# Optimization experiments

Measured on AMD Instinct MI355X. Metric: run time of the kernel, lower is better.

The kernel has to match this reference:

```python
import jax, jax.numpy as jnp
import numpy as np
from jax import lax

N, C_IN, H, W = 32, 128, 64, 64
C_OUT, KH, KW = 256, 3, 3
C_DIM = 64


def setup_inputs() -> dict:
    key = jax.random.key(0)
    k1, k2, k3, k4, k5 = jax.random.split(key, 5)
    return {
        "x": jax.random.normal(k1, (N, C_IN, H, W), dtype=jnp.float32),
        "c": jax.random.normal(k2, (N, C_DIM), dtype=jnp.float32),
        "weight": jax.random.normal(k3, (C_OUT, C_IN, KH, KW), dtype=jnp.float32),
        "c_weight": jax.random.normal(k4, (C_OUT, C_DIM), dtype=jnp.float32),
        "bias": jax.random.normal(k5, (C_OUT,), dtype=jnp.float32),
    }


def reference(x, c, weight, c_weight, bias):
    # Equivalent to the module's unfold + matmul path (groups=1, dilation=1,
    # zero padding=1, stride=1): a direct conv fused with the spatially
    # invariant context bias c @ c_weight^T and the channel bias.
    out = lax.conv_general_dilated(
        x, weight,
        window_strides=(1, 1),
        padding=((1, 1), (1, 1)),
        dimension_numbers=("NCHW", "OIHW", "NCHW"),
    )  # (N, C_out, H, W)
    ctx = jnp.einsum("nd,od->no", c, c_weight)  # (N, C_out), same at every spatial loc
    return out + ctx[:, :, None, None] + bias[None, :, None, None]
```

## Files before the change

kernel.cpp:

```cpp
#include <hip/hip_runtime.h>
#include <hip/hip_bf16.h>


#define NN   32
#define CIN  128
#define HH   64
#define WW   64
#define COUT 256
#define CDIM 64

#define WT_BYTES  ((size_t)9*COUT*CIN*2)
#define CTX_BYTES ((size_t)NN*COUT*4)
#define WS_NEEDED (WT_BYTES + CTX_BYTES)

#define AROWS 264
#define ARSTR 136
#define ACHNK 4488

typedef __attribute__((ext_vector_type(8))) short short8;
typedef __attribute__((ext_vector_type(4))) float float4v;

#define SETPRIO(x) __builtin_amdgcn_s_setprio(x)

__global__ __launch_bounds__(256) void prep_wc(const float* __restrict__ wgt,
                                               const float* __restrict__ c,
                                               const float* __restrict__ cw,
                                               const float* __restrict__ bias,
                                               __hip_bfloat16* __restrict__ wT,
                                               float* __restrict__ ctx) {
    int bid = blockIdx.x;
    if (bid < 1152) {
        int idx = bid * 256 + threadIdx.x;
        int ci  = idx & 127;
        int co  = (idx >> 7) & 255;
        int tap = idx >> 15;
        wT[idx] = __float2bfloat16(wgt[((size_t)co * CIN + ci) * 9 + tap]);
    } else {
        int idx = (bid - 1152) * 256 + threadIdx.x;
        int co = idx & 255, n = idx >> 8;
        float a = bias[co];
        #pragma unroll 8
        for (int d = 0; d < CDIM; ++d) a += c[n * CDIM + d] * cw[co * CDIM + d];
        ctx[idx] = a;
    }
}

__global__ __launch_bounds__(512, 4) void conv_mfma(
    const float* __restrict__ x,
    const __hip_bfloat16* __restrict__ wT,
    const float* __restrict__ ctx,
    float* __restrict__ out)
{
    __shared__ __align__(16) short A_s[AROWS * ARSTR];

    int bid = blockIdx.x;
    int mt  = (bid & 7) * 128 + (bid >> 3);
    int n   = mt >> 5;
    int h0  = (mt & 31) << 1;

    int tid  = threadIdx.x;
    int lane = tid & 63, wv = tid >> 6;
    int wm = (wv & 1) * 64;
    int wn = (wv >> 1) * 64;
    int l15 = lane & 15, lu = lane >> 4;

    const __hip_bfloat16* wB = wT + ((size_t)(wn + l15) * CIN) + lu * 8;

    short8 bCur[4], bNxt[4];
    #pragma unroll
    for (int ni = 0; ni < 4; ++ni)
        bCur[ni] = *(const short8*)(wB + (size_t)ni * (16 * CIN));

    #pragma unroll
    for (int z = 0; z < 9; ++z) {
        int g = z * 512 + tid;
        if (g < ACHNK) *(short8*)&A_s[g * 8] = (short8){};
    }
    __syncthreads();

    int h0m1 = h0 - 1;
    #pragma unroll
    for (int i = 0; i < 8; ++i) {
        int task = wv * 8 + i;
        int hl   = task >> 4;
        int oct  = task & 15;
        int hh   = h0m1 + hl;
        if (hh >= 0 && hh < HH) {
            const float* src = x + (((size_t)(n * CIN + oct * 8)) * HH + hh) * WW + lane;
            union { short8 s; __hip_bfloat16 b[8]; } u;
            #pragma unroll
            for (int k = 0; k < 8; ++k)
                u.b[k] = __float2bfloat16(src[(size_t)k * HH * WW]);
            int row = hl * 66 + 1 + lane;
            *(short8*)&A_s[row * ARSTR + ((oct) << 3) + 0] = u.s;
        }
    }
    __syncthreads();

    float4v acc[4][4] = {};
    int ohc = wm >> 6;

    for (int tap = 0; tap < 9; ++tap) {
        int kh  = (tap * 11) >> 5, kw = tap - kh * 3;
        int rb0 = (ohc + kh) * 66 + l15 + kw;
        #pragma unroll
        for (int kb = 0; kb < 4; ++kb) {
            int s1 = tap * 4 + kb + 1;
            if (s1 > 35) s1 = 0;
            int tap1 = s1 >> 2, kb1 = s1 & 3;
            const __hip_bfloat16* wNx = wB + (size_t)tap1 * (COUT * CIN) + kb1 * 32;
            #pragma unroll
            for (int ni = 0; ni < 4; ++ni)
                bNxt[ni] = *(const short8*)(wNx + (size_t)ni * (16 * CIN));

            int cL = kb * 4 + lu;
            short8 aF[4];
            #pragma unroll
            for (int mi = 0; mi < 4; ++mi) {
                int r = rb0 + mi * 16;
                aF[mi] = *(const short8*)&A_s[r * ARSTR + cL * 8];
            }

            SETPRIO(1);
            #pragma unroll
            for (int mi = 0; mi < 4; ++mi)
                #pragma unroll
                for (int ni = 0; ni < 4; ++ni)
                    acc[mi][ni] = __builtin_amdgcn_mfma_f32_16x16x32_bf16(
                        aF[mi], bCur[ni], acc[mi][ni], 0, 0, 0);
            SETPRIO(0);

            #pragma unroll
            for (int ni = 0; ni < 4; ++ni) bCur[ni] = bNxt[ni];
        }
    }

    #pragma unroll
    for (int ni = 0; ni < 4; ++ni) {
        int co = wn + ni * 16 + l15;
        float cv = ctx[n * COUT + co];
        float* ob = out + ((size_t)n * COUT + co) * (HH * WW);
        #pragma unroll
        for (int mi = 0; mi < 4; ++mi) {
            int rp = wm + mi * 16 + (lu << 2);
            int hh = h0 + (rp >> 6);
            int ww = rp & 63;
            float4v v = acc[mi][ni] + cv;
            *(float4v*)&ob[hh * WW + ww] = v;
        }
    }
}

__global__ __launch_bounds__(256) void contextual_conv_f32(
    const float* __restrict__ x, const float* __restrict__ c,
    const float* __restrict__ wgt, const float* __restrict__ cw,
    const float* __restrict__ bias, float* __restrict__ out)
{
    int idx = blockIdx.x * 256 + threadIdx.x;
    int w = idx & 63, h = (idx >> 6) & 63, cb = (idx >> 12) & 63, n = idx >> 18;
    float acc[4];
    #pragma unroll
    for (int j = 0; j < 4; ++j) acc[j] = bias[cb + j * 64];
    const float* cp = c + n * CDIM;
    for (int d = 0; d < CDIM; ++d) {
        float cv = cp[d];
        #pragma unroll
        for (int j = 0; j < 4; ++j) acc[j] += cv * cw[(cb + j * 64) * CDIM + d];
    }
    const float* xn = x + (size_t)n * (CIN * HH * WW);
    for (int ci = 0; ci < CIN; ++ci) {
        const float* xc = xn + ci * (HH * WW);
        float wv[4][9];
        #pragma unroll
        for (int j = 0; j < 4; ++j) {
            const float* wp = wgt + ((cb + j * 64) * CIN + ci) * 9;
            #pragma unroll
            for (int k = 0; k < 9; ++k) wv[j][k] = wp[k];
        }
        #pragma unroll
        for (int kh = 0; kh < 3; ++kh) {
            int hh = h + kh - 1;
            if (hh < 0 || hh >= HH) continue;
            const float* xr = xc + hh * WW;
            #pragma unroll
            for (int kw = 0; kw < 3; ++kw) {
                int ww = w + kw - 1;
                if (ww < 0 || ww >= WW) continue;
                float xv = xr[ww];
                #pragma unroll
                for (int j = 0; j < 4; ++j) acc[j] += xv * wv[j][kh * 3 + kw];
            }
        }
    }
    size_t obase = (size_t)n * (COUT * HH * WW) + (size_t)h * WW + w;
    #pragma unroll
    for (int j = 0; j < 4; ++j)
        out[obase + (size_t)(cb + j * 64) * (HH * WW)] = acc[j];
}

extern "C" void kernel_launch(void* const* d_in, const int* in_sizes, int n_in,
                              void* d_out, int out_size, void* d_ws, size_t ws_size,
                              hipStream_t stream) {
    const float* x    = (const float*)d_in[0];
    const float* c    = (const float*)d_in[1];
    const float* wgt  = (const float*)d_in[2];
    const float* cw   = (const float*)d_in[3];
    const float* bias = (const float*)d_in[4];
    float* out = (float*)d_out;

    if (ws_size < WS_NEEDED) {
        const int total_threads = NN * 64 * HH * WW;
        contextual_conv_f32<<<total_threads / 256, 256, 0, stream>>>(x, c, wgt, cw, bias, out);
        return;
    }

    char* ws = (char*)d_ws;
    __hip_bfloat16* wT = (__hip_bfloat16*)ws;
    float*          cx = (float*)(ws + WT_BYTES);

    prep_wc  <<<1184, 256, 0, stream>>>(wgt, c, cw, bias, wT, cx);
    conv_mfma<<<1024, 512, 0, stream>>>(x, wT, cx, out);
}
```

Baseline: 317.7 us.

## Double M-tile per block to four output rows and double-buffer weight fragments

Each block now computes four output rows instead of two, so each wave holds 8x4 MFMA accumulators and reuses each loaded weight fragment across twice as many A rows. The halo rows are loaded once per four rows rather than per two, which cuts redundant x loads and weight reads per output. Weight fragments are prefetched two k-steps ahead into a two-slot buffer, and the s_setprio hints are removed. In exchange, register and LDS use rise, occupancy drops (launch bounds now allow 2 blocks), and the grid halves to 512 blocks, which may underfill the GPU.

```diff
diff --git a/kernel.cpp b/kernel.cpp
--- a/kernel.cpp
+++ b/kernel.cpp
@@ -13,14 +13,12 @@
 #define CTX_BYTES ((size_t)NN*COUT*4)
 #define WS_NEEDED (WT_BYTES + CTX_BYTES)
 
-#define AROWS 264
+#define AROWS 396
 #define ARSTR 136
-#define ACHNK 4488
+#define ACHNK (AROWS*17)
 
 typedef __attribute__((ext_vector_type(8))) short short8;
 typedef __attribute__((ext_vector_type(4))) float float4v;
-
-#define SETPRIO(x) __builtin_amdgcn_s_setprio(x)
 
 __global__ __launch_bounds__(256) void prep_wc(const float* __restrict__ wgt,
                                                const float* __restrict__ c,
@@ -45,7 +43,7 @@
     }
 }
 
-__global__ __launch_bounds__(512, 4) void conv_mfma(
+__global__ __launch_bounds__(512, 2) void conv_mfma(
     const float* __restrict__ x,
     const __hip_bfloat16* __restrict__ wT,
     const float* __restrict__ ctx,
@@ -54,25 +52,27 @@
     __shared__ __align__(16) short A_s[AROWS * ARSTR];
 
     int bid = blockIdx.x;
-    int mt  = (bid & 7) * 128 + (bid >> 3);
-    int n   = mt >> 5;
-    int h0  = (mt & 31) << 1;
+    int mt  = (bid & 7) * 64 + (bid >> 3);
+    int n   = mt >> 4;
+    int h0  = (mt & 15) << 2;
 
     int tid  = threadIdx.x;
     int lane = tid & 63, wv = tid >> 6;
-    int wm = (wv & 1) * 64;
+    int wm = (wv & 1) * 128;
     int wn = (wv >> 1) * 64;
     int l15 = lane & 15, lu = lane >> 4;
 
     const __hip_bfloat16* wB = wT + ((size_t)(wn + l15) * CIN) + lu * 8;
 
-    short8 bCur[4], bNxt[4];
-    #pragma unroll
-    for (int ni = 0; ni < 4; ++ni)
-        bCur[ni] = *(const short8*)(wB + (size_t)ni * (16 * CIN));
-
-    #pragma unroll
-    for (int z = 0; z < 9; ++z) {
+    short8 bF[2][4];
+    #pragma unroll
+    for (int ni = 0; ni < 4; ++ni) {
+        bF[0][ni] = *(const short8*)(wB + (size_t)ni * (16 * CIN));
+        bF[1][ni] = *(const short8*)(wB + (size_t)ni * (16 * CIN) + 32);
+    }
+
+    #pragma unroll
+    for (int z = 0; z < 14; ++z) {
         int g = z * 512 + tid;
         if (g < ACHNK) *(short8*)&A_s[g * 8] = (short8){};
     }
@@ -80,8 +80,8 @@
 
     int h0m1 = h0 - 1;
     #pragma unroll
-    for (int i = 0; i < 8; ++i) {
-        int task = wv * 8 + i;
+    for (int i = 0; i < 12; ++i) {
+        int task = wv * 12 + i;
         int hl   = task >> 4;
         int oct  = task & 15;
         int hh   = h0m1 + hl;
@@ -92,12 +92,12 @@
             for (int k = 0; k < 8; ++k)
                 u.b[k] = __float2bfloat16(src[(size_t)k * HH * WW]);
             int row = hl * 66 + 1 + lane;
-            *(short8*)&A_s[row * ARSTR + ((oct) << 3) + 0] = u.s;
+            *(short8*)&A_s[row * ARSTR + (oct << 3)] = u.s;
         }
     }
     __syncthreads();
 
-    float4v acc[4][4] = {};
+    float4v acc[8][4] = {};
     int ohc = wm >> 6;
 
     for (int tap = 0; tap < 9; ++tap) {
@@ -105,33 +105,28 @@
         int rb0 = (ohc + kh) * 66 + l15 + kw;
         #pragma unroll
         for (int kb = 0; kb < 4; ++kb) {
-            int s1 = tap * 4 + kb + 1;
-            if (s1 > 35) s1 = 0;
-            int tap1 = s1 >> 2, kb1 = s1 & 3;
-            const __hip_bfloat16* wNx = wB + (size_t)tap1 * (COUT * CIN) + kb1 * 32;
-            #pragma unroll
-            for (int ni = 0; ni < 4; ++ni)
-                bNxt[ni] = *(const short8*)(wNx + (size_t)ni * (16 * CIN));
-
             int cL = kb * 4 + lu;
-            short8 aF[4];
-            #pragma unroll
-            for (int mi = 0; mi < 4; ++mi) {
-                int r = rb0 + mi * 16;
+            short8 aF[8];
+            #pragma unroll
+            for (int mi = 0; mi < 8; ++mi) {
+                int r = rb0 + (mi >> 2) * 66 + (mi & 3) * 16;
                 aF[mi] = *(const short8*)&A_s[r * ARSTR + cL * 8];
             }
 
-            SETPRIO(1);
-            #pragma unroll
-            for (int mi = 0; mi < 4; ++mi)
+            #pragma unroll
+            for (int mi = 0; mi < 8; ++mi)
                 #pragma unroll
                 for (int ni = 0; ni < 4; ++ni)
                     acc[mi][ni] = __builtin_amdgcn_mfma_f32_16x16x32_bf16(
-                        aF[mi], bCur[ni], acc[mi][ni], 0, 0, 0);
-            SETPRIO(0);
-
-            #pragma unroll
-            for (int ni = 0; ni < 4; ++ni) bCur[ni] = bNxt[ni];
+                        aF[mi], bF[kb & 1][ni], acc[mi][ni], 0, 0, 0);
+
+            int s2 = tap * 4 + kb + 2;
+            if (s2 > 35) s2 -= 36;
+            int tap2 = s2 >> 2, kb2 = s2 & 3;
+            const __hip_bfloat16* wNx = wB + (size_t)tap2 * (COUT * CIN) + kb2 * 32;
+            #pragma unroll
+            for (int ni = 0; ni < 4; ++ni)
+                bF[kb & 1][ni] = *(const short8*)(wNx + (size_t)ni * (16 * CIN));
         }
     }
 
@@ -141,7 +136,7 @@
         float cv = ctx[n * COUT + co];
         float* ob = out + ((size_t)n * COUT + co) * (HH * WW);
         #pragma unroll
-        for (int mi = 0; mi < 4; ++mi) {
+        for (int mi = 0; mi < 8; ++mi) {
             int rp = wm + mi * 16 + (lu << 2);
             int hh = h0 + (rp >> 6);
             int ww = rp & 63;
@@ -219,5 +214,5 @@
     float*          cx = (float*)(ws + WT_BYTES);
 
     prep_wc  <<<1184, 256, 0, stream>>>(wgt, c, cw, bias, wT, cx);
-    conv_mfma<<<1024, 512, 0, stream>>>(x, wT, cx, out);
-}
+    conv_mfma<<<512, 512, 0, stream>>>(x, wT, cx, out);
+}
```

Result: faster. 262.1 us (-17.5%).
